# Optimization experiments

Hardware: AMD Instinct MI355X
Metric: run time of the kernel (lower is better)

Reference implementation:

```python
import jax, jax.numpy as jnp
import numpy as np

B, CK, H, W = 1, 64, 30, 54
O, CV, M = 3, 512, 32400
TOP_K = 20


def setup_inputs() -> dict:
    key = jax.random.key(0)
    k1, k2, k3 = jax.random.split(key, 3)
    return {
        "qk": jax.random.normal(k1, (B, CK, H, W), dtype=jnp.float32),
        "mem_k": jax.random.normal(k2, (1, CK, M), dtype=jnp.float32),
        "mem_v": jax.random.normal(k3, (O, CV, M), dtype=jnp.float32),
        "top_k": TOP_K,
    }


def _softmax_w_top(aff, top_k):
    # aff: [B, M, Q]; top-k softmax over the memory axis M (dim=1), zeros elsewhere.
    b, m, q = aff.shape
    xt = aff.transpose(0, 2, 1)                      # [B, Q, M] -> top_k over last axis
    vals, idx = jax.lax.top_k(xt, top_k)             # [B, Q, K]
    soft = jax.nn.softmax(vals, axis=-1)             # stable softmax over the K kept entries
    w = jnp.zeros_like(xt).at[
        jnp.arange(b)[:, None, None],
        jnp.arange(q)[None, :, None],
        idx,
    ].set(soft)                                      # scatter back into [B, Q, M]
    return w.transpose(0, 2, 1)                      # [B, M, Q]


def reference(qk, mem_k, mem_v, top_k):
    b, ck, h, w = qk.shape
    q = h * w
    qk2 = qk.reshape(b, ck, q)                       # [B, CK, Q]
    mk = mem_k[0]                                    # [CK, M]
    a_sq = jnp.sum(mk * mk, axis=0)                  # [M]
    ab = jnp.einsum("cm,bcq->bmq", mk, qk2)          # [B, M, Q]
    scale = np.sqrt(ck).astype(np.float32)
    affinity = (2.0 * ab - a_sq[None, :, None]) / scale
    weights = _softmax_w_top(affinity, top_k)        # [B, M, Q] sparse (top_k nonzeros per column)
    readout = jnp.einsum("ocm,bmq->obcq", mem_v, weights)  # [O, B, CV, Q]
    o, _, cv, _ = readout.shape
    return readout.reshape(o, b, cv, h, q // h)      # [O, B, CV, H, W]
```

## Files before the change

### kernel.cpp

```cpp
#include <hip/hip_runtime.h>
#include <math.h>

#define M_TOT   32400
#define CKDIM   64
#define QTOT    1620
#define QPAD    1792
#define OCDIM   1536
#define TOPK    20
#define NSPLIT  81
#define MSPLIT  400
#define NTILES  25
#define KQUAD   3
#define KSPLIT  (4*KQUAD)
#define KEYSQ   (NSPLIT*KSPLIT)
#define POOL    32

typedef __attribute__((ext_vector_type(8))) short bf16x8;
typedef __attribute__((ext_vector_type(4))) float f32x4;

__device__ __forceinline__ float bf2f(unsigned short u) {
    union { unsigned int i; float f; } v;
    v.i = ((unsigned int)u) << 16;
    return v.f;
}

__device__ __forceinline__ unsigned short f2bf(float f) {
    union { float f; unsigned int i; } u;
    u.f = f;
    unsigned int r = u.i + 0x7FFF + ((u.i >> 16) & 1);
    return (unsigned short)(r >> 16);
}

__device__ __forceinline__ float med3f(float a, float b, float c) {
#if __has_builtin(__builtin_amdgcn_fmed3f)
    return __builtin_amdgcn_fmed3f(a, b, c);
#else
    return fmaxf(fminf(a, b), fminf(fmaxf(a, b), c));
#endif
}

#define INS3(t, x) do {                    \
    t[2] = med3f((x), t[1], t[2]);         \
    t[1] = med3f((x), t[0], t[1]);         \
    t[0] = fmaxf(t[0], (x));               \
} while (0)

#define INS8(t, x) do {                    \
    t[7] = med3f((x), t[6], t[7]);         \
    t[6] = med3f((x), t[5], t[6]);         \
    t[5] = med3f((x), t[4], t[5]);         \
    t[4] = med3f((x), t[3], t[4]);         \
    t[3] = med3f((x), t[2], t[3]);         \
    t[2] = med3f((x), t[1], t[2]);         \
    t[1] = med3f((x), t[0], t[1]);         \
    t[0] = fmaxf(t[0], (x));               \
} while (0)

__global__ __launch_bounds__(256) void k_prep(const float* __restrict__ mk,
                                              const float* __restrict__ qk,
                                              float* __restrict__ asq,
                                              unsigned short* __restrict__ mkT,
                                              float* __restrict__ mkTf,
                                              unsigned short* __restrict__ qkT,
                                              float* __restrict__ qkTf) {
    int idx = blockIdx.x * 256 + threadIdx.x;
    if (idx < M_TOT) {
        const int m = idx;
        float vals[CKDIM];
        float s = 0.f;
        #pragma unroll
        for (int c = 0; c < CKDIM; ++c) {
            vals[c] = mk[(size_t)c * M_TOT + m];
            s += vals[c] * vals[c];
        }
        asq[m] = s;
        uint4* db = (uint4*)(mkT + (size_t)m * CKDIM);
        #pragma unroll
        for (int g = 0; g < 8; ++g) {
            unsigned int r[4];
            #pragma unroll
            for (int p = 0; p < 4; ++p)
                r[p] = (unsigned int)f2bf(vals[g * 8 + 2 * p])
                     | ((unsigned int)f2bf(vals[g * 8 + 2 * p + 1]) << 16);
            db[g] = make_uint4(r[0], r[1], r[2], r[3]);
        }
        float4* df = (float4*)(mkTf + (size_t)m * CKDIM);
        #pragma unroll
        for (int g = 0; g < 16; ++g)
            df[g] = make_float4(vals[4 * g], vals[4 * g + 1], vals[4 * g + 2], vals[4 * g + 3]);
    } else if (idx < M_TOT + QPAD) {
        const int q = idx - M_TOT;
        float vals[CKDIM];
        #pragma unroll
        for (int c = 0; c < CKDIM; ++c)
            vals[c] = (q < QTOT) ? qk[(size_t)c * QTOT + q] : 0.f;
        uint4* db = (uint4*)(qkT + (size_t)q * CKDIM);
        #pragma unroll
        for (int g = 0; g < 8; ++g) {
            unsigned int r[4];
            #pragma unroll
            for (int p = 0; p < 4; ++p)
                r[p] = (unsigned int)f2bf(vals[g * 8 + 2 * p])
                     | ((unsigned int)f2bf(vals[g * 8 + 2 * p + 1]) << 16);
            db[g] = make_uint4(r[0], r[1], r[2], r[3]);
        }
        float4* df = (float4*)(qkTf + (size_t)q * CKDIM);
        #pragma unroll
        for (int g = 0; g < 16; ++g)
            df[g] = make_float4(vals[4 * g], vals[4 * g + 1], vals[4 * g + 2], vals[4 * g + 3]);
    }
}

__global__ __launch_bounds__(64) void k_topk_mfma(const unsigned short* __restrict__ mkT,
                                                  const unsigned short* __restrict__ qkT,
                                                  const float* __restrict__ asq,
                                                  float* __restrict__ pkeys) {
    const int lane = threadIdx.x;
    const int l15  = lane & 15;
    const int quad = lane >> 4;
    const int q_base = blockIdx.x * 64;
    const int sp     = blockIdx.y;
    const int m_base = sp * MSPLIT;

    bf16x8 bF[4][2];
    #pragma unroll
    for (int qt = 0; qt < 4; ++qt) {
        const unsigned short* p = qkT + (size_t)(q_base + qt * 16 + l15) * CKDIM + quad * 8;
        bF[qt][0] = *(const bf16x8*)(p);
        bF[qt][1] = *(const bf16x8*)(p + 32);
    }

    float key3[4][KQUAD];
    #pragma unroll
    for (int qt = 0; qt < 4; ++qt)
        #pragma unroll
        for (int j = 0; j < KQUAD; ++j) key3[qt][j] = -INFINITY;

    const unsigned short* pa = mkT + (size_t)(m_base + l15) * CKDIM + quad * 8;

    bf16x8 aF0 = *(const bf16x8*)(pa);
    bf16x8 aF1 = *(const bf16x8*)(pa + 32);
    f32x4  aq  = *(const f32x4*)(asq + m_base + quad * 4);

    for (int t = 0; t < NTILES; ++t) {
        bf16x8 nF0, nF1;
        f32x4  naq;
        if (t + 1 < NTILES) {
            const unsigned short* pn = pa + (size_t)(t + 1) * 1024;
            nF0 = *(const bf16x8*)(pn);
            nF1 = *(const bf16x8*)(pn + 32);
            naq = *(const f32x4*)(asq + m_base + (t + 1) * 16 + quad * 4);
        }
        f32x4 cinit = -0.5f * aq;
        const unsigned int mq = (unsigned int)(m_base + t * 16 + quad * 4);
        #pragma unroll
        for (int qt = 0; qt < 4; ++qt) {
            f32x4 c = cinit;
            c = __builtin_amdgcn_mfma_f32_16x16x32_bf16(aF0, bF[qt][0], c, 0, 0, 0);
            c = __builtin_amdgcn_mfma_f32_16x16x32_bf16(aF1, bF[qt][1], c, 0, 0, 0);
            #pragma unroll
            for (int i = 0; i < 4; ++i) {
                unsigned int kb = (__float_as_uint(c[i]) & 0xFFFF8000u) | (mq + i);
                float kf = __uint_as_float(kb);
                INS3(key3[qt], kf);
            }
        }
        aF0 = nF0; aF1 = nF1; aq = naq;
    }

    #pragma unroll
    for (int qt = 0; qt < 4; ++qt) {
        const int q = q_base + qt * 16 + l15;
        float* dst = pkeys + (size_t)q * KEYSQ + sp * KSPLIT + quad * KQUAD;
        #pragma unroll
        for (int j = 0; j < KQUAD; ++j) dst[j] = key3[qt][j];
    }
}

__global__ __launch_bounds__(64) void k_select(const float* __restrict__ pkeys,
                                               const float* __restrict__ mkTf,
                                               const float* __restrict__ qkTf,
                                               const float* __restrict__ asq,
                                               uint2* __restrict__ qw) {
    const int q    = blockIdx.x;
    const int lane = threadIdx.x;

    float t[8];
    #pragma unroll
    for (int j = 0; j < 8; ++j) t[j] = -INFINITY;
    const float* src = pkeys + (size_t)q * KEYSQ;
    #pragma unroll
    for (int i = 0; i < 16; ++i) {
        int s = lane + i * 64;
        float v = (s < KEYSQ) ? src[s] : -INFINITY;
        INS8(t, v);
    }

    float mykey = -INFINITY;
    for (int r = 0; r < POOL; ++r) {
        float h = t[0];
        float wm = h;
        #pragma unroll
        for (int off = 32; off; off >>= 1) wm = fmaxf(wm, __shfl_xor(wm, off));
        bool win = (h == wm);
        t[0] = win ? t[1] : t[0];
        t[1] = win ? t[2] : t[1];
        t[2] = win ? t[3] : t[2];
        t[3] = win ? t[4] : t[3];
        t[4] = win ? t[5] : t[4];
        t[5] = win ? t[6] : t[5];
        t[6] = win ? t[7] : t[6];
        t[7] = win ? -INFINITY : t[7];
        if (lane == r) mykey = wm;
    }

    const int  m_l = (int)(__float_as_uint(mykey) & 0x7FFFu);
    const bool act = (lane < POOL);

    const float4* rm = (const float4*)(mkTf + (size_t)m_l * CKDIM);
    const float4* rq = (const float4*)(qkTf + (size_t)q * CKDIM);
    float dot = 0.f;
    #pragma unroll
    for (int g = 0; g < 16; ++g) {
        float4 a = rm[g];
        float4 b = rq[g];
        dot += a.x * b.x + a.y * b.y + a.z * b.z + a.w * b.w;
    }
    float aff = act ? (2.f * dot - asq[m_l]) * 0.125f : -INFINITY;

    __shared__ float kv[TOPK];
    __shared__ int   ki[TOPK];

    for (int r = 0; r < TOPK; ++r) {
        float bv = aff;
        int   bm = m_l;
        #pragma unroll
        for (int off = 32; off; off >>= 1) {
            float ov = __shfl_xor(bv, off);
            int   om = __shfl_xor(bm, off);
            if (ov > bv || (ov == bv && om < bm)) { bv = ov; bm = om; }
        }
        if (aff == bv && m_l == bm) aff = -INFINITY;
        if (lane == 0) { kv[r] = bv; ki[r] = bm; }
    }
    __syncthreads();

    float e = (lane < TOPK) ? __expf(kv[lane] - kv[0]) : 0.f;
    float sum = e;
    #pragma unroll
    for (int off = 32; off; off >>= 1) sum += __shfl_xor(sum, off);

    if (lane < TOPK) {
        unsigned int wbits;
        { union { float f; unsigned int i; } u; u.f = e / sum; wbits = u.i; }
        qw[(size_t)q * TOPK + lane] = make_uint2((unsigned int)ki[lane], wbits);
    }
}

__global__ __launch_bounds__(512, 4) void k_readout(const float* __restrict__ mv,
                                                    const uint2* __restrict__ qw,
                                                    float* __restrict__ out) {
    __shared__ unsigned short row[M_TOT];
    const int oc  = blockIdx.x;
    const int tid = threadIdx.x;

    const uint4* s4 = (const uint4*)(mv + (size_t)oc * M_TOT);
    ushort4* d4 = (ushort4*)row;

    uint4 tA[8];
    #pragma unroll
    for (int it = 0; it < 8; ++it) tA[it] = s4[tid + it * 512];

    uint2 e0[TOPK];
    {
        const uint2* p0 = qw + (size_t)tid * TOPK;
        #pragma unroll
        for (int k = 0; k < TOPK; ++k) e0[k] = p0[k];
    }

    #pragma unroll
    for (int it = 0; it < 8; ++it) {
        uint4 v = tA[it];
        ushort4 h;
        h.x = f2bf(__uint_as_float(v.x));
        h.y = f2bf(__uint_as_float(v.y));
        h.z = f2bf(__uint_as_float(v.z));
        h.w = f2bf(__uint_as_float(v.w));
        d4[tid + it * 512] = h;
    }

    uint4 tB[7];
    #pragma unroll
    for (int it = 0; it < 7; ++it) tB[it] = s4[tid + (8 + it) * 512];
    uint4 tail;
    const int ti_idx = 15 * 512 + tid;
    if (tid < M_TOT / 4 - 15 * 512)
        tail = s4[ti_idx];

    #pragma unroll
    for (int it = 0; it < 7; ++it) {
        uint4 v = tB[it];
        ushort4 h;
        h.x = f2bf(__uint_as_float(v.x));
        h.y = f2bf(__uint_as_float(v.y));
        h.z = f2bf(__uint_as_float(v.z));
        h.w = f2bf(__uint_as_float(v.w));
        d4[tid + (8 + it) * 512] = h;
    }
    if (tid < M_TOT / 4 - 15 * 512) {
        ushort4 h;
        h.x = f2bf(__uint_as_float(tail.x));
        h.y = f2bf(__uint_as_float(tail.y));
        h.z = f2bf(__uint_as_float(tail.z));
        h.w = f2bf(__uint_as_float(tail.w));
        d4[ti_idx] = h;
    }
    __syncthreads();

    {
        float acc = 0.f;
        #pragma unroll
        for (int k = 0; k < TOPK; ++k)
            acc += __uint_as_float(e0[k].y) * bf2f(row[e0[k].x]);
        out[(size_t)oc * QTOT + tid] = acc;
    }
    #pragma unroll
    for (int j = 1; j < 4; ++j) {
        int q = tid + j * 512;
        if (q >= QTOT) break;
        const uint2* p = qw + (size_t)q * TOPK;
        float acc = 0.f;
        #pragma unroll
        for (int k = 0; k < TOPK; ++k) {
            uint2 e = p[k];
            acc += __uint_as_float(e.y) * bf2f(row[e.x]);
        }
        out[(size_t)oc * QTOT + q] = acc;
    }
}

extern "C" void kernel_launch(void* const* d_in, const int* in_sizes, int n_in,
                              void* d_out, int out_size, void* d_ws, size_t ws_size,
                              hipStream_t stream) {
    const float* qk = (const float*)d_in[0];
    const float* mk = (const float*)d_in[1];
    const float* mv = (const float*)d_in[2];
    float* out = (float*)d_out;

    char* ws = (char*)d_ws;
    float*          asq   = (float*)(ws);
    unsigned short* qkT   = (unsigned short*)(ws + 131072);
    unsigned short* mkT   = (unsigned short*)(ws + 360448);
    float*          mkTf  = (float*)(ws + 4507648);
    float*          qkTf  = (float*)(ws + 12802048);
    float*          pkeys = (float*)(ws + 13260800);
    uint2*          qw    = (uint2*)(ws + 20228096);

    k_prep     <<<dim3((M_TOT + QPAD + 255) / 256), dim3(256), 0, stream>>>(
                   mk, qk, asq, mkT, mkTf, qkT, qkTf);
    k_topk_mfma<<<dim3(28, NSPLIT),                 dim3(64),  0, stream>>>(mkT, qkT, asq, pkeys);
    k_select   <<<dim3(QTOT),                       dim3(64),  0, stream>>>(pkeys, mkTf, qkTf, asq, qw);
    k_readout  <<<dim3(OCDIM),                      dim3(512), 0, stream>>>(mv, qw, out);
}
```

Baseline: 355.7 us.

## Pack four waves per block, bitonic-sort select, simplify readout staging

The topk and select kernels now pack four independent 64-lane waves per 256-thread block instead of one wave per block, which cuts block count and scheduling overhead. The select kernel replaces 20 serial argmax shuffle rounds and shared-memory staging with a full 64-lane bitonic sort in registers, removing the __syncthreads. The readout kernel drops its prefetched weight registers and early split staging in favour of a simpler 3x5 load/convert loop. This lowers register pressure but gives up some of the load overlap the old code had.

```diff
diff --git a/kernel.cpp b/kernel.cpp
--- a/kernel.cpp
+++ b/kernel.cpp
@@ -111,14 +111,15 @@
     }
 }
 
-__global__ __launch_bounds__(64) void k_topk_mfma(const unsigned short* __restrict__ mkT,
-                                                  const unsigned short* __restrict__ qkT,
-                                                  const float* __restrict__ asq,
-                                                  float* __restrict__ pkeys) {
-    const int lane = threadIdx.x;
+__global__ __launch_bounds__(256) void k_topk_mfma(const unsigned short* __restrict__ mkT,
+                                                   const unsigned short* __restrict__ qkT,
+                                                   const float* __restrict__ asq,
+                                                   float* __restrict__ pkeys) {
+    const int lane = threadIdx.x & 63;
+    const int wave = threadIdx.x >> 6;
     const int l15  = lane & 15;
     const int quad = lane >> 4;
-    const int q_base = blockIdx.x * 64;
+    const int q_base = (blockIdx.x * 4 + wave) * 64;
     const int sp     = blockIdx.y;
     const int m_base = sp * MSPLIT;
 
@@ -177,13 +178,13 @@
     }
 }
 
-__global__ __launch_bounds__(64) void k_select(const float* __restrict__ pkeys,
-                                               const float* __restrict__ mkTf,
-                                               const float* __restrict__ qkTf,
-                                               const float* __restrict__ asq,
-                                               uint2* __restrict__ qw) {
-    const int q    = blockIdx.x;
-    const int lane = threadIdx.x;
+__global__ __launch_bounds__(256) void k_select(const float* __restrict__ pkeys,
+                                                const float* __restrict__ mkTf,
+                                                const float* __restrict__ qkTf,
+                                                const float* __restrict__ asq,
+                                                uint2* __restrict__ qw) {
+    const int q    = blockIdx.x * 4 + (threadIdx.x >> 6);
+    const int lane = threadIdx.x & 63;
 
     float t[8];
     #pragma unroll
@@ -228,24 +229,24 @@
     }
     float aff = act ? (2.f * dot - asq[m_l]) * 0.125f : -INFINITY;
 
-    __shared__ float kv[TOPK];
-    __shared__ int   ki[TOPK];
-
-    for (int r = 0; r < TOPK; ++r) {
-        float bv = aff;
-        int   bm = m_l;
-        #pragma unroll
-        for (int off = 32; off; off >>= 1) {
-            float ov = __shfl_xor(bv, off);
-            int   om = __shfl_xor(bm, off);
-            if (ov > bv || (ov == bv && om < bm)) { bv = ov; bm = om; }
-        }
-        if (aff == bv && m_l == bm) aff = -INFINITY;
-        if (lane == 0) { kv[r] = bv; ki[r] = bm; }
-    }
-    __syncthreads();
-
-    float e = (lane < TOPK) ? __expf(kv[lane] - kv[0]) : 0.f;
+    float v  = aff;
+    int   mi = m_l;
+    #pragma unroll
+    for (int k = 2; k <= 64; k <<= 1) {
+        #pragma unroll
+        for (int j = k >> 1; j > 0; j >>= 1) {
+            float ov = __shfl_xor(v, j);
+            int   om = __shfl_xor(mi, j);
+            const bool asc   = (lane & k) != 0;
+            const bool lower = (lane & j) == 0;
+            const bool gt    = (v > ov) || (v == ov && mi < om);
+            const bool keep  = lower ? (asc ? !gt : gt) : (asc ? gt : !gt);
+            if (!keep) { v = ov; mi = om; }
+        }
+    }
+
+    const float vmax = __shfl(v, 0);
+    float e = (lane < TOPK) ? __expf(v - vmax) : 0.f;
     float sum = e;
     #pragma unroll
     for (int off = 32; off; off >>= 1) sum += __shfl_xor(sum, off);
@@ -253,7 +254,7 @@
     if (lane < TOPK) {
         unsigned int wbits;
         { union { float f; unsigned int i; } u; u.f = e / sum; wbits = u.i; }
-        qw[(size_t)q * TOPK + lane] = make_uint2((unsigned int)ki[lane], wbits);
+        qw[(size_t)q * TOPK + lane] = make_uint2((unsigned int)mi, wbits);
     }
 }
 
@@ -267,65 +268,34 @@
     const uint4* s4 = (const uint4*)(mv + (size_t)oc * M_TOT);
     ushort4* d4 = (ushort4*)row;
 
-    uint4 tA[8];
-    #pragma unroll
-    for (int it = 0; it < 8; ++it) tA[it] = s4[tid + it * 512];
-
-    uint2 e0[TOPK];
-    {
-        const uint2* p0 = qw + (size_t)tid * TOPK;
-        #pragma unroll
-        for (int k = 0; k < TOPK; ++k) e0[k] = p0[k];
-    }
-
-    #pragma unroll
-    for (int it = 0; it < 8; ++it) {
-        uint4 v = tA[it];
+    #pragma unroll
+    for (int b = 0; b < 3; ++b) {
+        uint4 v[5];
+        #pragma unroll
+        for (int j = 0; j < 5; ++j) v[j] = s4[tid + (b * 5 + j) * 512];
+        #pragma unroll
+        for (int j = 0; j < 5; ++j) {
+            ushort4 h;
+            h.x = f2bf(__uint_as_float(v[j].x));
+            h.y = f2bf(__uint_as_float(v[j].y));
+            h.z = f2bf(__uint_as_float(v[j].z));
+            h.w = f2bf(__uint_as_float(v[j].w));
+            d4[tid + (b * 5 + j) * 512] = h;
+        }
+    }
+    if (tid < M_TOT / 4 - 15 * 512) {
+        uint4 v = s4[15 * 512 + tid];
         ushort4 h;
         h.x = f2bf(__uint_as_float(v.x));
         h.y = f2bf(__uint_as_float(v.y));
         h.z = f2bf(__uint_as_float(v.z));
         h.w = f2bf(__uint_as_float(v.w));
-        d4[tid + it * 512] = h;
-    }
-
-    uint4 tB[7];
-    #pragma unroll
-    for (int it = 0; it < 7; ++it) tB[it] = s4[tid + (8 + it) * 512];
-    uint4 tail;
-    const int ti_idx = 15 * 512 + tid;
-    if (tid < M_TOT / 4 - 15 * 512)
-        tail = s4[ti_idx];
-
-    #pragma unroll
-    for (int it = 0; it < 7; ++it) {
-        uint4 v = tB[it];
-        ushort4 h;
-        h.x = f2bf(__uint_as_float(v.x));
-        h.y = f2bf(__uint_as_float(v.y));
-        h.z = f2bf(__uint_as_float(v.z));
-        h.w = f2bf(__uint_as_float(v.w));
-        d4[tid + (8 + it) * 512] = h;
-    }
-    if (tid < M_TOT / 4 - 15 * 512) {
-        ushort4 h;
-        h.x = f2bf(__uint_as_float(tail.x));
-        h.y = f2bf(__uint_as_float(tail.y));
-        h.z = f2bf(__uint_as_float(tail.z));
-        h.w = f2bf(__uint_as_float(tail.w));
-        d4[ti_idx] = h;
+        d4[15 * 512 + tid] = h;
     }
     __syncthreads();
 
-    {
-        float acc = 0.f;
-        #pragma unroll
-        for (int k = 0; k < TOPK; ++k)
-            acc += __uint_as_float(e0[k].y) * bf2f(row[e0[k].x]);
-        out[(size_t)oc * QTOT + tid] = acc;
-    }
-    #pragma unroll
-    for (int j = 1; j < 4; ++j) {
+    #pragma unroll
+    for (int j = 0; j < 4; ++j) {
         int q = tid + j * 512;
         if (q >= QTOT) break;
         const uint2* p = qw + (size_t)q * TOPK;
@@ -358,7 +328,7 @@
 
     k_prep     <<<dim3((M_TOT + QPAD + 255) / 256), dim3(256), 0, stream>>>(
                    mk, qk, asq, mkT, mkTf, qkT, qkTf);
-    k_topk_mfma<<<dim3(28, NSPLIT),                 dim3(64),  0, stream>>>(mkT, qkT, asq, pkeys);
-    k_select   <<<dim3(QTOT),                       dim3(64),  0, stream>>>(pkeys, mkTf, qkTf, asq, qw);
+    k_topk_mfma<<<dim3(7, NSPLIT),                  dim3(256), 0, stream>>>(mkT, qkT, asq, pkeys);
+    k_select   <<<dim3(QTOT / 4),                   dim3(256), 0, stream>>>(pkeys, mkTf, qkTf, asq, qw);
     k_readout  <<<dim3(OCDIM),                      dim3(512), 0, stream>>>(mv, qw, out);
 }
```

Result: faster. 346.7 us (median of 2 runs) (-2.5%).
